# Kernel optimization log

Hardware: AMD Instinct MI355X
Metric: run time of the kernel (lower is better)

The kernel has to match this reference:

```python
import jax, jax.numpy as jnp
import numpy as np

N_QUBITS = 12
FAST_DEPTH = 4
FAST_DECAY = 0.9
LATENT = 512
BATCH = 2048


def _apply_ry(state, theta, wire):
    # state: (B, 2**n) real; RY is a real rotation. PennyLane default.qubit:
    # wire 0 is the most-significant bit of the state index.
    B = state.shape[0]
    s = state.reshape(B, 1 << wire, 2, -1)
    h = theta * 0.5
    c = jnp.cos(h)[:, None, None]
    sn = jnp.sin(h)[:, None, None]
    s0, s1 = s[:, :, 0], s[:, :, 1]
    out = jnp.stack([c * s0 - sn * s1, sn * s0 + c * s1], axis=2)
    return out.reshape(state.shape)


def _apply_cnot_adjacent(state, wire):
    # CNOT with control=wire, target=wire+1 (nearest-neighbor chain)
    B = state.shape[0]
    s = state.reshape(B, 1 << wire, 2, 2, -1)
    out = jnp.stack([s[:, :, 0], s[:, :, 1, ::-1]], axis=2)
    return out.reshape(state.shape)


def _fwp_circuit(x, fast, n_qubits, n_outputs):
    # x: (B, n_qubits) RY encoding angles; fast: (B, depth, n_qubits)
    B = x.shape[0]
    dim = 1 << n_qubits
    # Hadamard layer on |0...0> -> uniform positive real amplitudes.
    state = jnp.full((B, dim), 2.0 ** (-n_qubits / 2), dtype=x.dtype)
    for w in range(n_qubits):
        state = _apply_ry(state, x[:, w], w)
    for layer in range(fast.shape[1]):
        for w in range(n_qubits - 1):
            state = _apply_cnot_adjacent(state, w)
        for w in range(n_qubits):
            state = _apply_ry(state, fast[:, layer, w], w)
    probs = state * state  # real state -> |amp|^2
    outs = []
    for w in range(n_outputs):
        p = probs.reshape(B, 1 << w, 2, -1)
        outs.append(p[:, :, 0].sum(axis=(1, 2)) - p[:, :, 1].sum(axis=(1, 2)))
    return jnp.stack(outs, axis=1)  # (B, n_outputs) PauliZ expvals


def setup_inputs() -> dict:
    key = jax.random.key(0)
    ks = jax.random.split(key, 6)
    n, depth, latent = N_QUBITS, FAST_DEPTH, LATENT
    return {
        "x_t": jax.random.normal(ks[0], (BATCH, n), jnp.float32),
        "fast_prev": jax.random.normal(ks[1], (BATCH, depth, n), jnp.float32) * 0.1,
        "W_enc": jax.random.normal(ks[2], (latent, n), jnp.float32) / np.sqrt(n).astype(np.float32),
        "b_enc": jnp.zeros((latent,), jnp.float32),
        "W_upd": jax.random.normal(ks[3], (depth * n, latent), jnp.float32) / np.sqrt(latent).astype(np.float32),
        "b_upd": jnp.zeros((depth * n,), jnp.float32),
        "W_ro": jax.random.normal(ks[4], (1, n), jnp.float32) / np.sqrt(n).astype(np.float32),
        "b_ro": jnp.zeros((1,), jnp.float32),
    }


def reference(x_t, fast_prev, W_enc, b_enc, W_upd, b_upd, W_ro, b_ro):
    latent = jnp.tanh(x_t @ W_enc.T + b_enc)
    delta = (latent @ W_upd.T + b_upd).reshape(x_t.shape[0], FAST_DEPTH, N_QUBITS)
    fast_next = FAST_DECAY * fast_prev + delta
    q_out = _fwp_circuit(x_t, fast_next, N_QUBITS, N_QUBITS)  # n_outputs = n_qubits
    y_t = q_out @ W_ro.T + b_ro
    return (y_t, fast_next)
```

## Files before the change

kernel.cpp:

```cpp
#include <hip/hip_runtime.h>

static constexpr int NQ    = 12;
static constexpr int DEPTH = 4;
static constexpr int LAT   = 512;
static constexpr int FAST  = DEPTH * NQ;
static constexpr float DECAY = 0.9f;
static constexpr int P     = 68;

using v2f = __attribute__((ext_vector_type(2))) float;


template<int S, int B>
__device__ __forceinline__ void bfly_half(float (&v)[64], float c, float s) {
    v2f c2 = {c, c}, s2 = {s, s};
    #pragma unroll
    for (int r0 = B; r0 < B + 32; r0 += 2) {
        if ((r0 & S) == 0) {
            v2f a = {v[r0],     v[r0 + 1]};
            v2f b = {v[r0 + S], v[r0 + S + 1]};
            v2f na = c2 * a - s2 * b;
            v2f nb = s2 * a + c2 * b;
            v[r0]     = na.x;  v[r0 + 1]     = na.y;
            v[r0 + S] = nb.x;  v[r0 + S + 1] = nb.y;
        }
    }
}

template<int B>
__device__ __forceinline__ void bfly1_half(float (&v)[64], float c, float s) {
    v2f cs = {c, s}, nsc = {-s, c};
    #pragma unroll
    for (int r0 = B; r0 < B + 32; r0 += 2) {
        float a = v[r0], b = v[r0 + 1];
        v2f aa = {a, a}, bb = {b, b};
        v2f res = cs * aa + nsc * bb;
        v[r0]     = res.x;
        v[r0 + 1] = res.y;
    }
}

template<int B>
__device__ __forceinline__ void ry5_half(float (&v)[64], const v2f* cs) {
    bfly_half<16, B>(v, cs[0].x, cs[0].y);
    bfly_half<8,  B>(v, cs[1].x, cs[1].y);
    bfly_half<4,  B>(v, cs[2].x, cs[2].y);
    bfly_half<2,  B>(v, cs[3].x, cs[3].y);
    bfly1_half<B>(v, cs[4].x, cs[4].y);
}

__device__ __forceinline__ void bfly32(float (&v)[64], float c, float s) {
    v2f c2 = {c, c}, s2 = {s, s};
    #pragma unroll
    for (int r0 = 0; r0 < 32; r0 += 2) {
        v2f a = {v[r0],      v[r0 + 1]};
        v2f b = {v[r0 + 32], v[r0 + 33]};
        v2f na = c2 * a - s2 * b;
        v2f nb = s2 * a + c2 * b;
        v[r0]      = na.x;  v[r0 + 1]  = na.y;
        v[r0 + 32] = nb.x;  v[r0 + 33] = nb.y;
    }
}

__device__ __forceinline__ void ry6(float (&v)[64], const v2f* cs) {
    ry5_half<0>(v, cs + 1);
    ry5_half<32>(v, cs + 1);
    bfly32(v, cs[0].x, cs[0].y);
}

__device__ __forceinline__ void p1w(const float (&v)[64], float* X, int lane) {
    #pragma unroll
    for (int k = 0; k < 16; k++)
        *(float4*)&X[lane * P + 4 * k] =
            (float4){v[4 * k], v[4 * k + 1], v[4 * k + 2], v[4 * k + 3]};
}
__device__ __forceinline__ void p1r(float (&v)[64], const float* X, int A0, int A1) {
    #pragma unroll
    for (int r = 0; r < 64; r++) {
        const int g = r ^ (r >> 1);
        v[r] = X[g * P + ((r & 1) ? A1 : A0)];
    }
}
__device__ __forceinline__ void p2w(const float (&v)[64], float* X, int lane) {
    #pragma unroll
    for (int q = 0; q < 64; q++) X[q * P + lane] = v[q];
}
__device__ __forceinline__ void p2r(float (&v)[64], const float* X, int lane) {
    #pragma unroll
    for (int k = 0; k < 16; k++) {
        float4 t = *(const float4*)&X[lane * P + 4 * k];
        v[4 * k]     = t.x;  v[4 * k + 1] = t.y;
        v[4 * k + 2] = t.z;  v[4 * k + 3] = t.w;
    }
}

__device__ __forceinline__ void init_state(float (&v)[64], const float (&xa)[NQ], int lane) {
    float g0[NQ], g1[NQ];
    #pragma unroll
    for (int w = 0; w < NQ; w++) {
        float hh = 0.5f * xa[w];
        float c = __cosf(hh), s = __sinf(hh);
        g0[w] = (c - s) * 0.70710678118654752f;
        g1[w] = (c + s) * 0.70710678118654752f;
    }
    float L = 1.0f;
    #pragma unroll
    for (int w = 0; w < 6; w++)
        L *= ((lane >> (5 - w)) & 1) ? g1[w] : g0[w];
    v[0] = L;
    #pragma unroll
    for (int w = 6; w < NQ; w++) {
        const int S = 1 << (11 - w);
        #pragma unroll
        for (int r = 0; r < 64; r += 2 * S) {
            v[r + S] = v[r] * g1[w];
            v[r]     = v[r] * g0[w];
        }
    }
}

__global__ __launch_bounds__(64, 1)
void fwp_kernel(const float* __restrict__ x_t,
                const float* __restrict__ fast_prev,
                const float* __restrict__ W_enc,
                const float* __restrict__ b_enc,
                const float* __restrict__ W_upd,
                const float* __restrict__ b_upd,
                const float* __restrict__ W_ro,
                const float* __restrict__ b_ro,
                float* __restrict__ out_y,
                float* __restrict__ out_fast) {
    const int lane = threadIdx.x;
    const int e    = blockIdx.x;

    __shared__ __align__(16) float X[64 * P];
    __shared__ __align__(8)  v2f   cs[FAST];

    float* lat = X;

    float xa[NQ];
    #pragma unroll
    for (int k = 0; k < NQ; k++) xa[k] = x_t[e * NQ + k];

    {
        const float4* we = (const float4*)(W_enc + lane * 8 * NQ);
        float4 be0 = *(const float4*)&b_enc[8 * lane];
        float4 be1 = *(const float4*)&b_enc[8 * lane + 4];
        float be[8] = {be0.x, be0.y, be0.z, be0.w, be1.x, be1.y, be1.z, be1.w};
        float l[8];
        #pragma unroll
        for (int t = 0; t < 8; t++) {
            float4 a0 = we[3 * t], a1 = we[3 * t + 1], a2 = we[3 * t + 2];
            float s = be[t]
                + a0.x * xa[0] + a0.y * xa[1] + a0.z * xa[2]  + a0.w * xa[3]
                + a1.x * xa[4] + a1.y * xa[5] + a1.z * xa[6]  + a1.w * xa[7]
                + a2.x * xa[8] + a2.y * xa[9] + a2.z * xa[10] + a2.w * xa[11];
            l[t] = tanhf(s);
        }
        *(float4*)&lat[8 * lane]     = (float4){l[0], l[1], l[2], l[3]};
        *(float4*)&lat[8 * lane + 4] = (float4){l[4], l[5], l[6], l[7]};
    }

    if (lane < FAST) {
        const float4* wr = (const float4*)(W_upd + lane * LAT);
        const float4* la = (const float4*)(lat);
        float s = b_upd[lane];
        #pragma unroll 8
        for (int j = 0; j < LAT / 4; j++) {
            float4 w4 = wr[j];
            float4 a4 = la[j];
            s += w4.x * a4.x + w4.y * a4.y + w4.z * a4.z + w4.w * a4.w;
        }
        float ang = DECAY * fast_prev[e * FAST + lane] + s;
        out_fast[e * FAST + lane] = ang;
        cs[lane] = (v2f){__cosf(0.5f * ang), __sinf(0.5f * ang)};
    }

    float v[64];
    init_state(v, xa, lane);

    const int A0 = ((lane ^ (lane >> 1)) & 31) | (lane & 32);
    const int A1 = A0 ^ 32;

    #pragma unroll 1
    for (int layer = 0; layer < DEPTH; layer++) {
        v2f c[NQ];
        #pragma unroll
        for (int w = 0; w < NQ; w++) c[w] = cs[layer * NQ + w];

        p1w(v, X, lane);
        p1r(v, X, A0, A1);
        ry6(v, c);

        p2w(v, X, lane);
        p2r(v, X, lane);
        ry6(v, c + 6);
    }

    float wro[NQ];
    #pragma unroll
    for (int w = 0; w < NQ; w++) wro[w] = W_ro[w];
    float sl = 0.0f;
    #pragma unroll
    for (int w = 0; w < 6; w++)
        sl += ((lane >> (5 - w)) & 1) ? -wro[w] : wro[w];

    float tot = 0.0f, pw[6] = {0, 0, 0, 0, 0, 0};
    #pragma unroll
    for (int r = 0; r < 64; r++) {
        float p = v[r] * v[r];
        tot += p;
        pw[0] += (r & 32) ? -p : p;
        pw[1] += (r & 16) ? -p : p;
        pw[2] += (r & 8)  ? -p : p;
        pw[3] += (r & 4)  ? -p : p;
        pw[4] += (r & 2)  ? -p : p;
        pw[5] += (r & 1)  ? -p : p;
    }
    float y = sl * tot;
    #pragma unroll
    for (int k = 0; k < 6; k++) y += wro[6 + k] * pw[k];
    #pragma unroll
    for (int m = 32; m >= 1; m >>= 1) y += __shfl_xor(y, m, 64);
    if (lane == 0) out_y[e] = y + b_ro[0];
}

extern "C" void kernel_launch(void* const* d_in, const int* in_sizes, int n_in,
                              void* d_out, int out_size, void* d_ws, size_t ws_size,
                              hipStream_t stream) {
    const float* x_t       = (const float*)d_in[0];
    const float* fast_prev = (const float*)d_in[1];
    const float* W_enc     = (const float*)d_in[2];
    const float* b_enc     = (const float*)d_in[3];
    const float* W_upd     = (const float*)d_in[4];
    const float* b_upd     = (const float*)d_in[5];
    const float* W_ro      = (const float*)d_in[6];
    const float* b_ro      = (const float*)d_in[7];
    float* out = (float*)d_out;

    fwp_kernel<<<2048, 64, 0, stream>>>(x_t, fast_prev, W_enc, b_enc,
                                        W_upd, b_upd, W_ro, b_ro,
                                        out , out + 2048 );
}
```

Before: 114.7 us.

## Replace LDS transposes with cross-lane permutes for qubit rotations

```diff
diff --git a/kernel.cpp b/kernel.cpp
--- a/kernel.cpp
+++ b/kernel.cpp
@@ -5,10 +5,29 @@
 static constexpr int LAT   = 512;
 static constexpr int FAST  = DEPTH * NQ;
 static constexpr float DECAY = 0.9f;
-static constexpr int P     = 68;
 
 using v2f = __attribute__((ext_vector_type(2))) float;
 
+
+__device__ __forceinline__ constexpr int G6(int x){ return (x ^ (x >> 1)) & 63; }
+
+__device__ __forceinline__ float bperm(int idx, float v){
+    return __int_as_float(__builtin_amdgcn_ds_bpermute(idx, __float_as_int(v)));
+}
+template<int CTRL>
+__device__ __forceinline__ float dppf(float x){
+    return __int_as_float(__builtin_amdgcn_mov_dpp(__float_as_int(x), CTRL, 0xF, 0xF, false));
+}
+__device__ __forceinline__ float xsum32(float x){
+    float a = x, b = x;
+    asm("v_permlane32_swap_b32 %0, %1" : "+v"(a), "+v"(b));
+    return a + b;
+}
+__device__ __forceinline__ float xsum16(float x){
+    float a = x, b = x;
+    asm("v_permlane16_swap_b32 %0, %1" : "+v"(a), "+v"(b));
+    return a + b;
+}
 
 template<int S, int B>
 __device__ __forceinline__ void bfly_half(float (&v)[64], float c, float s) {
@@ -25,7 +44,6 @@
         }
     }
 }
-
 template<int B>
 __device__ __forceinline__ void bfly1_half(float (&v)[64], float c, float s) {
     v2f cs = {c, s}, nsc = {-s, c};
@@ -38,7 +56,6 @@
         v[r0 + 1] = res.y;
     }
 }
-
 template<int B>
 __device__ __forceinline__ void ry5_half(float (&v)[64], const v2f* cs) {
     bfly_half<16, B>(v, cs[0].x, cs[0].y);
@@ -47,7 +64,6 @@
     bfly_half<2,  B>(v, cs[3].x, cs[3].y);
     bfly1_half<B>(v, cs[4].x, cs[4].y);
 }
-
 __device__ __forceinline__ void bfly32(float (&v)[64], float c, float s) {
     v2f c2 = {c, c}, s2 = {s, s};
     #pragma unroll
@@ -60,37 +76,10 @@
         v[r0 + 32] = nb.x;  v[r0 + 33] = nb.y;
     }
 }
-
 __device__ __forceinline__ void ry6(float (&v)[64], const v2f* cs) {
     ry5_half<0>(v, cs + 1);
     ry5_half<32>(v, cs + 1);
     bfly32(v, cs[0].x, cs[0].y);
-}
-
-__device__ __forceinline__ void p1w(const float (&v)[64], float* X, int lane) {
-    #pragma unroll
-    for (int k = 0; k < 16; k++)
-        *(float4*)&X[lane * P + 4 * k] =
-            (float4){v[4 * k], v[4 * k + 1], v[4 * k + 2], v[4 * k + 3]};
-}
-__device__ __forceinline__ void p1r(float (&v)[64], const float* X, int A0, int A1) {
-    #pragma unroll
-    for (int r = 0; r < 64; r++) {
-        const int g = r ^ (r >> 1);
-        v[r] = X[g * P + ((r & 1) ? A1 : A0)];
-    }
-}
-__device__ __forceinline__ void p2w(const float (&v)[64], float* X, int lane) {
-    #pragma unroll
-    for (int q = 0; q < 64; q++) X[q * P + lane] = v[q];
-}
-__device__ __forceinline__ void p2r(float (&v)[64], const float* X, int lane) {
-    #pragma unroll
-    for (int k = 0; k < 16; k++) {
-        float4 t = *(const float4*)&X[lane * P + 4 * k];
-        v[4 * k]     = t.x;  v[4 * k + 1] = t.y;
-        v[4 * k + 2] = t.z;  v[4 * k + 3] = t.w;
-    }
 }
 
 __device__ __forceinline__ void init_state(float (&v)[64], const float (&xa)[NQ], int lane) {
@@ -104,12 +93,12 @@
     }
     float L = 1.0f;
     #pragma unroll
-    for (int w = 0; w < 6; w++)
-        L *= ((lane >> (5 - w)) & 1) ? g1[w] : g0[w];
+    for (int w = 6; w < NQ; w++)
+        L *= ((lane >> (11 - w)) & 1) ? g1[w] : g0[w];
     v[0] = L;
     #pragma unroll
-    for (int w = 6; w < NQ; w++) {
-        const int S = 1 << (11 - w);
+    for (int w = 0; w < 6; w++) {
+        const int S = 32 >> w;
         #pragma unroll
         for (int r = 0; r < 64; r += 2 * S) {
             v[r + S] = v[r] * g1[w];
@@ -132,10 +121,8 @@
     const int lane = threadIdx.x;
     const int e    = blockIdx.x;
 
-    __shared__ __align__(16) float X[64 * P];
+    __shared__ __align__(16) float lat[LAT];
     __shared__ __align__(8)  v2f   cs[FAST];
-
-    float* lat = X;
 
     float xa[NQ];
     #pragma unroll
@@ -175,11 +162,14 @@
         cs[lane] = (v2f){__cosf(0.5f * ang), __sinf(0.5f * ang)};
     }
 
-    float v[64];
-    init_state(v, xa, lane);
-
-    const int A0 = ((lane ^ (lane >> 1)) & 31) | (lane & 32);
-    const int A1 = A0 ^ 32;
+    float u[64];
+    init_state(u, xa, lane);
+
+    const int idxA = G6(lane) * 4;
+    const int idxB = idxA ^ 128;
+
+    #define SIG1(h, src) { const int idx_ = ((h) & 1) ? idxB : idxA; \
+        u[h] = bperm(idx_, (src)); }
 
     #pragma unroll 1
     for (int layer = 0; layer < DEPTH; layer++) {
@@ -187,27 +177,86 @@
         #pragma unroll
         for (int w = 0; w < NQ; w++) c[w] = cs[layer * NQ + w];
 
-        p1w(v, X, lane);
-        p1r(v, X, A0, A1);
-        ry6(v, c);
-
-        p2w(v, X, lane);
-        p2r(v, X, lane);
-        ry6(v, c + 6);
-    }
+        SIG1(0, u[0]);  SIG1(1, u[1]);
+        { float t = u[2]; SIG1(2, u[3]); SIG1(3, t); }
+        { float t = u[4]; SIG1(4, u[6]);  SIG1(6, u[5]);  SIG1(5, u[7]);  SIG1(7, t); }
+        { float t = u[8]; SIG1(8, u[12]); SIG1(12, u[10]); SIG1(10, u[15]); SIG1(15, t); }
+        { float t = u[9]; SIG1(9, u[13]); SIG1(13, u[11]); SIG1(11, u[14]); SIG1(14, t); }
+        { float t = u[16]; SIG1(16, u[24]); SIG1(24, u[20]); SIG1(20, u[30]); SIG1(30, u[17]);
+                           SIG1(17, u[25]); SIG1(25, u[21]); SIG1(21, u[31]); SIG1(31, t); }
+        { float t = u[18]; SIG1(18, u[27]); SIG1(27, u[22]); SIG1(22, u[29]); SIG1(29, u[19]);
+                           SIG1(19, u[26]); SIG1(26, u[23]); SIG1(23, u[28]); SIG1(28, t); }
+        { float t = u[32]; SIG1(32, u[48]); SIG1(48, u[40]); SIG1(40, u[60]); SIG1(60, u[34]);
+                           SIG1(34, u[51]); SIG1(51, u[42]); SIG1(42, u[63]); SIG1(63, t); }
+        { float t = u[33]; SIG1(33, u[49]); SIG1(49, u[41]); SIG1(41, u[61]); SIG1(61, u[35]);
+                           SIG1(35, u[50]); SIG1(50, u[43]); SIG1(43, u[62]); SIG1(62, t); }
+        { float t = u[36]; SIG1(36, u[54]); SIG1(54, u[45]); SIG1(45, u[59]); SIG1(59, u[38]);
+                           SIG1(38, u[53]); SIG1(53, u[47]); SIG1(47, u[56]); SIG1(56, t); }
+        { float t = u[37]; SIG1(37, u[55]); SIG1(55, u[44]); SIG1(44, u[58]); SIG1(58, u[39]);
+                           SIG1(39, u[52]); SIG1(52, u[46]); SIG1(46, u[57]); SIG1(57, t); }
+
+        {
+            float sv = (lane & 32) ? c[6].y : -c[6].y;
+            float cm = c[6].x - sv;
+            #pragma unroll
+            for (int h = 0; h < 64; h++)
+                u[h] = __builtin_fmaf(cm, u[h], sv * xsum32(u[h]));
+        }
+        {
+            float sv = (lane & 16) ? c[7].y : -c[7].y;
+            float cm = c[7].x - sv;
+            #pragma unroll
+            for (int h = 0; h < 64; h++)
+                u[h] = __builtin_fmaf(cm, u[h], sv * xsum16(u[h]));
+        }
+        {
+            float sv = (lane & 8) ? c[8].y : -c[8].y;
+            #pragma unroll
+            for (int h = 0; h < 64; h++) {
+                float p = dppf<0x128>(u[h]);
+                u[h] = __builtin_fmaf(c[8].x, u[h], sv * p);
+            }
+        }
+        {
+            float sv = (lane & 4) ? c[9].y : -c[9].y;
+            #pragma unroll
+            for (int h = 0; h < 64; h++) {
+                float p = dppf<0x141>(dppf<0x1B>(u[h]));
+                u[h] = __builtin_fmaf(c[9].x, u[h], sv * p);
+            }
+        }
+        {
+            float sv = (lane & 2) ? c[10].y : -c[10].y;
+            #pragma unroll
+            for (int h = 0; h < 64; h++) {
+                float p = dppf<0x4E>(u[h]);
+                u[h] = __builtin_fmaf(c[10].x, u[h], sv * p);
+            }
+        }
+        {
+            float sv = (lane & 1) ? c[11].y : -c[11].y;
+            #pragma unroll
+            for (int h = 0; h < 64; h++) {
+                float p = dppf<0xB1>(u[h]);
+                u[h] = __builtin_fmaf(c[11].x, u[h], sv * p);
+            }
+        }
+        ry6(u, c);
+    }
+    #undef SIG1
 
     float wro[NQ];
     #pragma unroll
     for (int w = 0; w < NQ; w++) wro[w] = W_ro[w];
     float sl = 0.0f;
     #pragma unroll
-    for (int w = 0; w < 6; w++)
-        sl += ((lane >> (5 - w)) & 1) ? -wro[w] : wro[w];
+    for (int w = 6; w < NQ; w++)
+        sl += ((lane >> (11 - w)) & 1) ? -wro[w] : wro[w];
 
     float tot = 0.0f, pw[6] = {0, 0, 0, 0, 0, 0};
     #pragma unroll
     for (int r = 0; r < 64; r++) {
-        float p = v[r] * v[r];
+        float p = u[r] * u[r];
         tot += p;
         pw[0] += (r & 32) ? -p : p;
         pw[1] += (r & 16) ? -p : p;
@@ -218,7 +267,7 @@
     }
     float y = sl * tot;
     #pragma unroll
-    for (int k = 0; k < 6; k++) y += wro[6 + k] * pw[k];
+    for (int k = 0; k < 6; k++) y += wro[k] * pw[k];
     #pragma unroll
     for (int m = 32; m >= 1; m >>= 1) y += __shfl_xor(y, m, 64);
     if (lane == 0) out_y[e] = y + b_ro[0];
```

After: 124.4 us. 8.5% more time.
